# Kernel tuning notes

Measured on AMD Instinct MI355X. Metric: run time of the kernel, lower is better.

The kernel has to match this reference:

```python
import jax, jax.numpy as jnp
import numpy as np

H = 16  # num_heads
EPS_DEN = 1e-6


def setup_inputs() -> dict:
    key = jax.random.key(0)
    k1, k2, k3 = jax.random.split(key, 3)
    x = jax.random.normal(k1, (2, 4096, 2048), dtype=jnp.float32)
    # torch Linear weights stored as [in, out] so y = x @ W
    w_qkv = jax.random.normal(k2, (2048, 6144), dtype=jnp.float32) * 0.02
    w_out = jax.random.normal(k3, (2048, 2048), dtype=jnp.float32) * 0.02
    decay_param = jnp.full((H,), 0.95, dtype=jnp.float32)
    return {"x": x, "w_qkv": w_qkv, "w_out": w_out, "decay_param": decay_param}


def _decay_scan(x, decay, init):
    """Inclusive causal scan: s_t = decay * s_{t-1} + x_t, s_{-1} = init.
    x: [B,H,T,D], decay: [1,H,1], init: [B,H,D] -> [B,H,T,D].
    (Numerically stable recurrence form; identical math to the torch
    decay-weighted cumsum closed form.)"""
    xT = jnp.moveaxis(x, 2, 0)  # [T,B,H,D]

    def step(s, xt):
        s = decay * s + xt  # decay [1,H,1] broadcasts over [B,H,D]
        return s, s

    _, ys = jax.lax.scan(step, init, xT)
    return jnp.moveaxis(ys, 0, 2)  # [B,H,T,D]


def _phi(z):
    return jax.nn.elu(z) + 1.0


def reference(x, w_qkv, w_out, decay_param):
    B, T, Hid = x.shape
    D = Hid // H
    qkv = x @ w_qkv  # [B,T,3*Hid]
    q, k, v = jnp.split(qkv, 3, axis=-1)

    def to_bhtd(t):
        return t.reshape(B, T, H, D).transpose(0, 2, 1, 3)

    q = _phi(to_bhtd(q))
    k = _phi(to_bhtd(k))
    v = to_bhtd(v)

    decay = jax.nn.sigmoid(decay_param).reshape(1, H, 1)  # per-head decay in (0,1)
    init = jnp.zeros((B, H, D), dtype=x.dtype)

    running_kv = _decay_scan(k * v, decay, init)  # [B,H,T,D]
    running_ksum = _decay_scan(k, decay, init)    # [B,H,T,D]

    den = jnp.clip(jnp.sum(q * running_ksum, axis=-1, keepdims=True), EPS_DEN, None)
    out = q * running_kv / den  # [B,H,T,D]
    out = out.transpose(0, 2, 1, 3).reshape(B, T, Hid) @ w_out

    new_kv = running_kv[:, :, -1, :]
    new_ksum = running_ksum[:, :, -1, :]
    return out, new_kv, new_ksum
```

## Files before the change

kernel.cpp:

```cpp
#include <hip/hip_runtime.h>
#include <hip/hip_bf16.h>
#include <stdint.h>

constexpr int NB = 2;
constexpr int NT = 4096;
constexpr int NH = 16;
constexpr int ND = 128;
constexpr int HID = NH * ND;
constexpr int QKV_N = 3 * HID;
constexpr int ROWS = NB * NT;
constexpr int CHUNK = 64;
constexpr int NCH = NT / CHUNK;

typedef __bf16 bf16x8 __attribute__((ext_vector_type(8)));
typedef float  f32x4  __attribute__((ext_vector_type(4)));

__device__ inline unsigned short f2bf(float f) {
    unsigned u = __builtin_bit_cast(unsigned, f);
    u += 0x7fffu + ((u >> 16) & 1u);
    return (unsigned short)(u >> 16);
}
__device__ inline float bf2f(unsigned short b) {
    unsigned u = ((unsigned)b) << 16;
    return __builtin_bit_cast(float, u);
}

__global__ void cast_kernel(const float* __restrict__ in,
                            unsigned short* __restrict__ out, size_t n4) {
    size_t i = blockIdx.x * (size_t)blockDim.x + threadIdx.x;
    size_t stride = (size_t)gridDim.x * blockDim.x;
    for (; i < n4; i += stride) {
        float4 v = reinterpret_cast<const float4*>(in)[i];
        ushort4 o;
        o.x = f2bf(v.x); o.y = f2bf(v.y); o.z = f2bf(v.z); o.w = f2bf(v.w);
        reinterpret_cast<ushort4*>(out)[i] = o;
    }
}

__global__ __launch_bounds__(256) void transpose_cast(
        const float* __restrict__ in, unsigned short* __restrict__ out,
        int R, int Cn) {
    __shared__ float tile[32][33];
    const int c  = threadIdx.x & 31;
    const int r8 = threadIdx.x >> 5;
    const int r0 = blockIdx.y * 32, c0 = blockIdx.x * 32;
    #pragma unroll
    for (int i = 0; i < 32; i += 8)
        tile[r8 + i][c] = in[(size_t)(r0 + r8 + i) * Cn + c0 + c];
    __syncthreads();
    #pragma unroll
    for (int i = 0; i < 32; i += 8)
        out[(size_t)(c0 + r8 + i) * R + r0 + c] = f2bf(tile[c][r8 + i]);
}


__device__ __forceinline__ void gll(const unsigned short* src, unsigned short* dst) {
    __builtin_amdgcn_global_load_lds(
        (const __attribute__((address_space(1))) void*)src,
        (__attribute__((address_space(3))) void*)dst, 16, 0, 0);
}

__device__ __forceinline__ void stage_t(const unsigned short* G, int K, int k0,
                                        unsigned short* lds, int wid, int lane) {
    const int rbase = wid * 32;
    const int rl = lane >> 3;
    const int ce = ((lane & 7) ^ rl) * 8;
    #pragma unroll
    for (int j = 0; j < 4; ++j) {
        gll(G + (size_t)(rbase + j * 8 + rl) * K + k0 + ce,
            lds + (rbase + j * 8) * 64);
    }
}

__device__ __forceinline__ bf16x8 ld_frag(const unsigned short* tile,
                                          int r, int kk, int fq) {
    int slot = (kk * 4 + fq) ^ (r & 7);
    return *reinterpret_cast<const bf16x8*>(tile + r * 64 + slot * 8);
}

template <typename OUT_T>
__global__ __launch_bounds__(256, 2) void gemm128(
        const unsigned short* __restrict__ A,
        const unsigned short* __restrict__ Bt,
        OUT_T* __restrict__ C,
        int M, int N, int K, int byc) {
    __shared__ unsigned short As0[128 * 64];
    __shared__ unsigned short As1[128 * 64];
    __shared__ unsigned short Bs0[128 * 64];
    __shared__ unsigned short Bs1[128 * 64];

    const int bid = blockIdx.x;
    const int xcd = bid & 7;
    const int c   = bid >> 3;
    const int by  = xcd * byc + (c % byc);
    const int bx  = c / byc;
    const int tid = threadIdx.x, wid = tid >> 6, lane = tid & 63;
    const int wm  = wid >> 1, wn = wid & 1;
    const int fr  = lane & 15, fq = lane >> 4;

    const unsigned short* Ag = A  + (size_t)by * 128 * K;
    const unsigned short* Bg = Bt + (size_t)bx * 128 * K;

    f32x4 acc[4][4] = {};

    stage_t(Ag, K, 0, As0, wid, lane);
    stage_t(Bg, K, 0, Bs0, wid, lane);
    __syncthreads();

    const int NK = K / 64;
    for (int t = 0; t < NK; ++t) {
        const unsigned short* Ac = (t & 1) ? As1 : As0;
        const unsigned short* Bc = (t & 1) ? Bs1 : Bs0;
        if (t + 1 < NK) {
            unsigned short* An = (t & 1) ? As0 : As1;
            unsigned short* Bn = (t & 1) ? Bs0 : Bs1;
            stage_t(Ag, K, (t + 1) * 64, An, wid, lane);
            stage_t(Bg, K, (t + 1) * 64, Bn, wid, lane);
        }
        bf16x8 af[4][2], bf[4][2];
        #pragma unroll
        for (int m = 0; m < 4; ++m) {
            int r = wm * 64 + m * 16 + fr;
            af[m][0] = ld_frag(Ac, r, 0, fq);
            af[m][1] = ld_frag(Ac, r, 1, fq);
        }
        #pragma unroll
        for (int n = 0; n < 4; ++n) {
            int r = wn * 64 + n * 16 + fr;
            bf[n][0] = ld_frag(Bc, r, 0, fq);
            bf[n][1] = ld_frag(Bc, r, 1, fq);
        }
        __builtin_amdgcn_s_setprio(1);
        #pragma unroll
        for (int kk = 0; kk < 2; ++kk)
            #pragma unroll
            for (int m = 0; m < 4; ++m)
                #pragma unroll
                for (int n = 0; n < 4; ++n)
                    acc[m][n] = __builtin_amdgcn_mfma_f32_16x16x32_bf16(
                        af[m][kk], bf[n][kk], acc[m][n], 0, 0, 0);
        __builtin_amdgcn_s_setprio(0);
        __syncthreads();
    }

    const int bm = by * 128, bn = bx * 128;
    #pragma unroll
    for (int m = 0; m < 4; ++m) {
        #pragma unroll
        for (int n = 0; n < 4; ++n) {
            #pragma unroll
            for (int r = 0; r < 4; ++r) {
                int row = bm + wm * 64 + m * 16 + fq * 4 + r;
                int col = bn + wn * 64 + n * 16 + fr;
                float v = acc[m][n][r];
                if constexpr (sizeof(OUT_T) == 2)
                    C[(size_t)row * N + col] = (OUT_T)f2bf(v);
                else
                    C[(size_t)row * N + col] = (OUT_T)v;
            }
        }
    }
}

__device__ inline float phi_f(float z) { return z > 0.f ? z + 1.f : __expf(z); }
__device__ inline float sigmoid_f(float z) { return 1.f / (1.f + __expf(-z)); }

__global__ void scan_pass1(const unsigned short* __restrict__ qkv,
                           const float* __restrict__ decay_param,
                           float* __restrict__ fkv, float* __restrict__ fk) {
    const int blk = blockIdx.x;
    const int c = blk % NCH;
    const int h = (blk / NCH) % NH;
    const int b = blk / (NCH * NH);
    const int lane = threadIdx.x;
    const float dec = sigmoid_f(decay_param[h]);

    float skv0 = 0.f, skv1 = 0.f, sk0 = 0.f, sk1 = 0.f;
    const unsigned short* base =
        qkv + ((size_t)b * NT + (size_t)c * CHUNK) * QKV_N + h * ND;
    for (int t = 0; t < CHUNK; ++t) {
        const unsigned short* r = base + (size_t)t * QKV_N;
        unsigned kp = *reinterpret_cast<const unsigned*>(r + HID + 2 * lane);
        unsigned vp = *reinterpret_cast<const unsigned*>(r + 2 * HID + 2 * lane);
        float k0 = phi_f(bf2f((unsigned short)(kp & 0xffff)));
        float k1 = phi_f(bf2f((unsigned short)(kp >> 16)));
        float v0 = bf2f((unsigned short)(vp & 0xffff));
        float v1 = bf2f((unsigned short)(vp >> 16));
        skv0 = fmaf(dec, skv0, k0 * v0);
        skv1 = fmaf(dec, skv1, k1 * v1);
        sk0  = fmaf(dec, sk0,  k0);
        sk1  = fmaf(dec, sk1,  k1);
    }
    size_t o = (size_t)blk * ND + 2 * lane;
    *reinterpret_cast<float2*>(&fkv[o]) = make_float2(skv0, skv1);
    *reinterpret_cast<float2*>(&fk[o])  = make_float2(sk0, sk1);
}

__global__ void scan_pass2(const float* __restrict__ fkv, const float* __restrict__ fk,
                           const float* __restrict__ decay_param,
                           float* __restrict__ ckv, float* __restrict__ ck,
                           float* __restrict__ out_states) {
    const int bh = blockIdx.x;
    const int h = bh % NH;
    const int lane = threadIdx.x;
    const float dec = sigmoid_f(decay_param[h]);
    const float dL = powf(dec, (float)CHUNK);

    float Skv0 = 0.f, Skv1 = 0.f, Sk0 = 0.f, Sk1 = 0.f;
    for (int c = 0; c < NCH; ++c) {
        size_t o = ((size_t)bh * NCH + c) * ND + 2 * lane;
        *reinterpret_cast<float2*>(&ckv[o]) = make_float2(Skv0, Skv1);
        *reinterpret_cast<float2*>(&ck[o])  = make_float2(Sk0, Sk1);
        float2 fv = *reinterpret_cast<const float2*>(&fkv[o]);
        float2 fs = *reinterpret_cast<const float2*>(&fk[o]);
        Skv0 = fmaf(dL, Skv0, fv.x);
        Skv1 = fmaf(dL, Skv1, fv.y);
        Sk0  = fmaf(dL, Sk0,  fs.x);
        Sk1  = fmaf(dL, Sk1,  fs.y);
    }
    size_t so = (size_t)bh * ND + 2 * lane;
    *reinterpret_cast<float2*>(&out_states[so]) = make_float2(Skv0, Skv1);
    *reinterpret_cast<float2*>(&out_states[NB * NH * ND + so]) = make_float2(Sk0, Sk1);
}

__global__ void scan_pass3(const unsigned short* __restrict__ qkv,
                           const float* __restrict__ decay_param,
                           const float* __restrict__ ckv, const float* __restrict__ ck,
                           unsigned short* __restrict__ attn) {
    const int blk = blockIdx.x;
    const int c = blk % NCH;
    const int h = (blk / NCH) % NH;
    const int b = blk / (NCH * NH);
    const int lane = threadIdx.x;
    const float dec = sigmoid_f(decay_param[h]);

    size_t co = (size_t)blk * ND + 2 * lane;
    float2 cv = *reinterpret_cast<const float2*>(&ckv[co]);
    float2 cs = *reinterpret_cast<const float2*>(&ck[co]);
    float skv0 = cv.x, skv1 = cv.y, sk0 = cs.x, sk1 = cs.y;

    const unsigned short* base =
        qkv + ((size_t)b * NT + (size_t)c * CHUNK) * QKV_N + h * ND;
    unsigned short* abase =
        attn + ((size_t)b * NT + (size_t)c * CHUNK) * HID + h * ND;

    for (int t = 0; t < CHUNK; ++t) {
        const unsigned short* r = base + (size_t)t * QKV_N;
        unsigned qp = *reinterpret_cast<const unsigned*>(r + 2 * lane);
        unsigned kp = *reinterpret_cast<const unsigned*>(r + HID + 2 * lane);
        unsigned vp = *reinterpret_cast<const unsigned*>(r + 2 * HID + 2 * lane);
        float q0 = phi_f(bf2f((unsigned short)(qp & 0xffff)));
        float q1 = phi_f(bf2f((unsigned short)(qp >> 16)));
        float k0 = phi_f(bf2f((unsigned short)(kp & 0xffff)));
        float k1 = phi_f(bf2f((unsigned short)(kp >> 16)));
        float v0 = bf2f((unsigned short)(vp & 0xffff));
        float v1 = bf2f((unsigned short)(vp >> 16));
        skv0 = fmaf(dec, skv0, k0 * v0);
        skv1 = fmaf(dec, skv1, k1 * v1);
        sk0  = fmaf(dec, sk0,  k0);
        sk1  = fmaf(dec, sk1,  k1);
        float den = fmaf(q0, sk0, q1 * sk1);
        #pragma unroll
        for (int m = 1; m < 64; m <<= 1) den += __shfl_xor(den, m, 64);
        den = fmaxf(den, 1e-6f);
        float inv = 1.f / den;
        unsigned o = ((unsigned)f2bf(q1 * skv1 * inv) << 16) |
                     (unsigned)f2bf(q0 * skv0 * inv);
        *reinterpret_cast<unsigned*>(abase + (size_t)t * HID + 2 * lane) = o;
    }
}

extern "C" void kernel_launch(void* const* d_in, const int* in_sizes, int n_in,
                              void* d_out, int out_size, void* d_ws, size_t ws_size,
                              hipStream_t stream) {
    const float* x      = (const float*)d_in[0];
    const float* w_qkv  = (const float*)d_in[1];
    const float* w_out  = (const float*)d_in[2];
    const float* decayp = (const float*)d_in[3];
    float* out = (float*)d_out;

    char* ws = (char*)d_ws;
    unsigned short* xb     = (unsigned short*)ws;
    unsigned short* wqkvT  = xb    + (size_t)ROWS * HID;
    unsigned short* woutT  = wqkvT + (size_t)QKV_N * HID;
    unsigned short* qkvb   = woutT + (size_t)HID * HID;
    unsigned short* attnb  = qkvb  + (size_t)ROWS * QKV_N;
    float* fkv = (float*)(attnb + (size_t)ROWS * HID);
    float* fk  = fkv + (size_t)NB * NH * NCH * ND;
    float* ckv = fk  + (size_t)NB * NH * NCH * ND;
    float* ck  = ckv + (size_t)NB * NH * NCH * ND;

    cast_kernel<<<2048, 256, 0, stream>>>(x, xb, (size_t)ROWS * HID / 4);
    dim3 tg1(QKV_N / 32, HID / 32);
    transpose_cast<<<tg1, 256, 0, stream>>>(w_qkv, wqkvT, HID, QKV_N);
    dim3 tg2(HID / 32, HID / 32);
    transpose_cast<<<tg2, 256, 0, stream>>>(w_out, woutT, HID, HID);

    {
        int nby = ROWS / 128, nbx = QKV_N / 128;
        gemm128<unsigned short><<<nby * nbx, 256, 0, stream>>>(
            xb, wqkvT, qkvb, ROWS, QKV_N, HID, nby / 8);
    }

    scan_pass1<<<NB * NH * NCH, 64, 0, stream>>>(qkvb, decayp, fkv, fk);
    scan_pass2<<<NB * NH, 64, 0, stream>>>(fkv, fk, decayp, ckv, ck,
                                           out + (size_t)ROWS * HID);
    scan_pass3<<<NB * NH * NCH, 64, 0, stream>>>(qkvb, decayp, ckv, ck, attnb);

    {
        int nby = ROWS / 128, nbx = HID / 128;
        gemm128<float><<<nby * nbx, 256, 0, stream>>>(
            attnb, woutT, out, ROWS, HID, HID, nby / 8);
    }
}
```

Baseline: 354.2 us.

## Load GEMM B fragments directly from global and fuse prep kernels

The three cast/transpose kernels are merged into one launch. The GEMM also stops staging B tiles through LDS: each wave reads its B fragments straight from global memory, which halves shared memory use, and launch bounds are raised to allow four blocks per CU. The goal is higher occupancy and less LDS traffic and synchronisation, at the cost of uncoalesced, unpipelined global loads for B, with each 16-byte row fragment strided by K.

After: 1.005 ms. +183.8%, slower.

```diff
diff --git a/kernel.cpp b/kernel.cpp
--- a/kernel.cpp
+++ b/kernel.cpp
@@ -25,25 +25,41 @@
     return __builtin_bit_cast(float, u);
 }
 
-__global__ void cast_kernel(const float* __restrict__ in,
-                            unsigned short* __restrict__ out, size_t n4) {
-    size_t i = blockIdx.x * (size_t)blockDim.x + threadIdx.x;
-    size_t stride = (size_t)gridDim.x * blockDim.x;
-    for (; i < n4; i += stride) {
-        float4 v = reinterpret_cast<const float4*>(in)[i];
-        ushort4 o;
-        o.x = f2bf(v.x); o.y = f2bf(v.y); o.z = f2bf(v.z); o.w = f2bf(v.w);
-        reinterpret_cast<ushort4*>(out)[i] = o;
-    }
-}
-
-__global__ __launch_bounds__(256) void transpose_cast(
-        const float* __restrict__ in, unsigned short* __restrict__ out,
-        int R, int Cn) {
+constexpr int PREP_CAST_BLK = 2048;
+constexpr int PREP_TQ_BLK   = (QKV_N / 32) * (HID / 32);
+constexpr int PREP_TW_BLK   = (HID / 32) * (HID / 32);
+
+__global__ __launch_bounds__(256) void prep_kernel(
+        const float* __restrict__ x, const float* __restrict__ w_qkv,
+        const float* __restrict__ w_out,
+        unsigned short* __restrict__ xb, unsigned short* __restrict__ wqkvT,
+        unsigned short* __restrict__ woutT) {
     __shared__ float tile[32][33];
+    const int b = blockIdx.x;
+    if (b < PREP_CAST_BLK) {
+        size_t n4 = (size_t)ROWS * HID / 4;
+        size_t i = b * (size_t)blockDim.x + threadIdx.x;
+        size_t stride = (size_t)PREP_CAST_BLK * blockDim.x;
+        for (; i < n4; i += stride) {
+            float4 v = reinterpret_cast<const float4*>(x)[i];
+            ushort4 o;
+            o.x = f2bf(v.x); o.y = f2bf(v.y); o.z = f2bf(v.z); o.w = f2bf(v.w);
+            reinterpret_cast<ushort4*>(xb)[i] = o;
+        }
+        return;
+    }
+    const float* in;
+    unsigned short* out;
+    int R, Cn, tb;
+    if (b < PREP_CAST_BLK + PREP_TQ_BLK) {
+        tb = b - PREP_CAST_BLK; in = w_qkv; out = wqkvT; R = HID; Cn = QKV_N;
+    } else {
+        tb = b - PREP_CAST_BLK - PREP_TQ_BLK; in = w_out; out = woutT; R = HID; Cn = HID;
+    }
+    const int nbx = Cn / 32;
+    const int c0 = (tb % nbx) * 32, r0 = (tb / nbx) * 32;
     const int c  = threadIdx.x & 31;
     const int r8 = threadIdx.x >> 5;
-    const int r0 = blockIdx.y * 32, c0 = blockIdx.x * 32;
     #pragma unroll
     for (int i = 0; i < 32; i += 8)
         tile[r8 + i][c] = in[(size_t)(r0 + r8 + i) * Cn + c0 + c];
@@ -79,15 +95,13 @@
 }
 
 template <typename OUT_T>
-__global__ __launch_bounds__(256, 2) void gemm128(
+__global__ __launch_bounds__(256, 4) void gemm128(
         const unsigned short* __restrict__ A,
         const unsigned short* __restrict__ Bt,
         OUT_T* __restrict__ C,
         int M, int N, int K, int byc) {
     __shared__ unsigned short As0[128 * 64];
     __shared__ unsigned short As1[128 * 64];
-    __shared__ unsigned short Bs0[128 * 64];
-    __shared__ unsigned short Bs1[128 * 64];
 
     const int bid = blockIdx.x;
     const int xcd = bid & 7;
@@ -101,34 +115,33 @@
     const unsigned short* Ag = A  + (size_t)by * 128 * K;
     const unsigned short* Bg = Bt + (size_t)bx * 128 * K;
 
+    const unsigned short* Bl = Bg + (size_t)(wn * 64 + fr) * K + fq * 8;
+
     f32x4 acc[4][4] = {};
 
     stage_t(Ag, K, 0, As0, wid, lane);
-    stage_t(Bg, K, 0, Bs0, wid, lane);
     __syncthreads();
 
     const int NK = K / 64;
     for (int t = 0; t < NK; ++t) {
         const unsigned short* Ac = (t & 1) ? As1 : As0;
-        const unsigned short* Bc = (t & 1) ? Bs1 : Bs0;
         if (t + 1 < NK) {
             unsigned short* An = (t & 1) ? As0 : As1;
-            unsigned short* Bn = (t & 1) ? Bs0 : Bs1;
             stage_t(Ag, K, (t + 1) * 64, An, wid, lane);
-            stage_t(Bg, K, (t + 1) * 64, Bn, wid, lane);
         }
-        bf16x8 af[4][2], bf[4][2];
+        bf16x8 bf[4][2];
+        #pragma unroll
+        for (int n = 0; n < 4; ++n)
+            #pragma unroll
+            for (int kk = 0; kk < 2; ++kk)
+                bf[n][kk] = *reinterpret_cast<const bf16x8*>(
+                    Bl + (size_t)(n * 16) * K + t * 64 + kk * 32);
+        bf16x8 af[4][2];
         #pragma unroll
         for (int m = 0; m < 4; ++m) {
             int r = wm * 64 + m * 16 + fr;
             af[m][0] = ld_frag(Ac, r, 0, fq);
             af[m][1] = ld_frag(Ac, r, 1, fq);
-        }
-        #pragma unroll
-        for (int n = 0; n < 4; ++n) {
-            int r = wn * 64 + n * 16 + fr;
-            bf[n][0] = ld_frag(Bc, r, 0, fq);
-            bf[n][1] = ld_frag(Bc, r, 1, fq);
         }
         __builtin_amdgcn_s_setprio(1);
         #pragma unroll
@@ -290,11 +303,8 @@
     float* ckv = fk  + (size_t)NB * NH * NCH * ND;
     float* ck  = ckv + (size_t)NB * NH * NCH * ND;
 
-    cast_kernel<<<2048, 256, 0, stream>>>(x, xb, (size_t)ROWS * HID / 4);
-    dim3 tg1(QKV_N / 32, HID / 32);
-    transpose_cast<<<tg1, 256, 0, stream>>>(w_qkv, wqkvT, HID, QKV_N);
-    dim3 tg2(HID / 32, HID / 32);
-    transpose_cast<<<tg2, 256, 0, stream>>>(w_out, woutT, HID, HID);
+    prep_kernel<<<PREP_CAST_BLK + PREP_TQ_BLK + PREP_TW_BLK, 256, 0, stream>>>(
+        x, w_qkv, w_out, xb, wqkvT, woutT);
 
     {
         int nby = ROWS / 128, nbx = QKV_N / 128;
```
